# Kernel tuning notes

Measured on AMD Instinct MI355X. Metric: run time of the kernel, lower is better.

The kernel has to match this reference:

```python
import jax, jax.numpy as jnp
import numpy as np

N_NODES = 50000
N_EDGES = 1600000
D = 128


def setup_inputs() -> dict:
    key = jax.random.key(0)
    k1, k2, k3, k4 = jax.random.split(key, 4)
    x = jax.random.normal(k1, (N_NODES, D), dtype=jnp.float32)
    src = jax.random.randint(k2, (N_EDGES,), 0, N_NODES, dtype=jnp.int64)
    dst = jax.random.randint(k3, (N_EDGES,), 0, N_NODES, dtype=jnp.int64)
    # Linear(2*D, 1): weight [2*D, 1] (transposed vs torch), bias [1]
    W = jax.random.normal(k4, (2 * D, 1), dtype=jnp.float32) * (1.0 / np.sqrt(2 * D))
    b = jnp.zeros((1,), dtype=jnp.float32)
    return {"x": x, "src": src, "dst": dst, "W": W, "b": b}


def reference(x, src, dst, W, b):
    # score_e = W^T [x[src_e]; x[dst_e]] + b
    # Equivalent split form avoids materializing the [E, 2D] concat when possible,
    # but stays mathematically identical to cat + Linear.
    Ws, Wd = W[:D], W[D:]            # [D,1] each
    xs = x @ Ws                       # [N,1] per-node src contribution
    xd = x @ Wd                       # [N,1] per-node dst contribution
    score = xs[src] + xd[dst] + b     # [E,1]
    return score
```

## Files before the change

### kernel.cpp

```cpp
#include <hip/hip_runtime.h>
#include <hip/hip_bf16.h>

#define DDIM 128
#define K2_BLOCKS 256
#define K2_THREADS 1024
#define MAX_TAB32 25088

typedef float vf4 __attribute__((ext_vector_type(4)));
typedef int   vi4 __attribute__((ext_vector_type(4)));

__device__ __forceinline__ float bf16_to_f32(unsigned short u) {
    return __uint_as_float(((unsigned int)u) << 16);
}

__global__ __launch_bounds__(256) void node_proj_kernel(
    const float* __restrict__ x,
    const float* __restrict__ W,
    __hip_bfloat16* __restrict__ xs,
    __hip_bfloat16* __restrict__ xd,
    int n_nodes)
{
    const int tib    = threadIdx.x;
    const int lane   = tib & 63;
    const int wid    = blockIdx.x * (256 / 64) + (tib >> 6);
    const int nwaves = gridDim.x * (256 / 64);
    const int lc     = lane & 31;
    const int half   = lane >> 5;

    const vf4 ws4 = *reinterpret_cast<const vf4*>(W + lc * 4);
    const vf4 wd4 = *reinterpret_cast<const vf4*>(W + DDIM + lc * 4);

    const int npairs = n_nodes >> 1;
    for (int p = wid; p < npairs; p += nwaves) {
        const int row = 2 * p + half;
        const vf4 xv = __builtin_nontemporal_load(
            reinterpret_cast<const vf4*>(x + (size_t)row * DDIM + lc * 4));
        float s = xv.x * ws4.x + xv.y * ws4.y + xv.z * ws4.z + xv.w * ws4.w;
        float d = xv.x * wd4.x + xv.y * wd4.y + xv.z * wd4.z + xv.w * wd4.w;
        #pragma unroll
        for (int m = 16; m >= 1; m >>= 1) {
            s += __shfl_xor(s, m, 64);
            d += __shfl_xor(d, m, 64);
        }
        if (lc == 0) {
            xs[row] = __float2bfloat16(s);
            xd[row] = __float2bfloat16(d);
        }
    }
    if ((n_nodes & 1) && wid == 0 && half == 0) {
        const int row = n_nodes - 1;
        const vf4 xv = *reinterpret_cast<const vf4*>(
            x + (size_t)row * DDIM + lc * 4);
        float s = xv.x * ws4.x + xv.y * ws4.y + xv.z * ws4.z + xv.w * ws4.w;
        float d = xv.x * wd4.x + xv.y * wd4.y + xv.z * wd4.z + xv.w * wd4.w;
        #pragma unroll
        for (int m = 16; m >= 1; m >>= 1) {
            s += __shfl_xor(s, m, 64);
            d += __shfl_xor(d, m, 64);
        }
        if (lc == 0) {
            xs[row] = __float2bfloat16(s);
            xd[row] = __float2bfloat16(d);
        }
    }
}

__global__ __launch_bounds__(K2_THREADS) void edge_lds_kernel(
    const int* __restrict__ src,
    const int* __restrict__ dst,
    const unsigned int* __restrict__ xs32,
    const unsigned int* __restrict__ xd32,
    const float* __restrict__ b,
    float* __restrict__ out,
    int n_nodes, int n_quads, int n_edges)
{
    __shared__ unsigned short tab[MAX_TAB32 * 2];
    unsigned int* tab32 = reinterpret_cast<unsigned int*>(tab);

    const int tid = threadIdx.x;
    const int gid = blockIdx.x * K2_THREADS + tid;
    const int T   = K2_BLOCKS * K2_THREADS;
    const int n32 = (n_nodes + 1) >> 1;
    const float bb = b[0];

    for (int i = tid; i < n32; i += K2_THREADS) tab32[i] = xs32[i];
    __syncthreads();

    const int q0 = gid, q1 = gid + T;
    const bool h0 = q0 < n_quads, h1 = q1 < n_quads;
    vi4 t0 = {0,0,0,0}, t1 = {0,0,0,0};
    vf4 p0 = {0,0,0,0}, p1 = {0,0,0,0};
    if (h0) {
        const vi4 s = __builtin_nontemporal_load(
            reinterpret_cast<const vi4*>(src) + q0);
        t0 = __builtin_nontemporal_load(
            reinterpret_cast<const vi4*>(dst) + q0);
        p0.x = bf16_to_f32(tab[s.x]) + bb;
        p0.y = bf16_to_f32(tab[s.y]) + bb;
        p0.z = bf16_to_f32(tab[s.z]) + bb;
        p0.w = bf16_to_f32(tab[s.w]) + bb;
    }
    if (h1) {
        const vi4 s = __builtin_nontemporal_load(
            reinterpret_cast<const vi4*>(src) + q1);
        t1 = __builtin_nontemporal_load(
            reinterpret_cast<const vi4*>(dst) + q1);
        p1.x = bf16_to_f32(tab[s.x]) + bb;
        p1.y = bf16_to_f32(tab[s.y]) + bb;
        p1.z = bf16_to_f32(tab[s.z]) + bb;
        p1.w = bf16_to_f32(tab[s.w]) + bb;
    }
    const int tail = n_edges & 3;
    int te = -1; float pt = 0.f; int td = 0;
    if (blockIdx.x == 0 && tid < tail) {
        te = (n_quads << 2) + tid;
        td = dst[te];
        pt = bf16_to_f32(tab[src[te]]) + bb;
    }

    __syncthreads();
    for (int i = tid; i < n32; i += K2_THREADS) tab32[i] = xd32[i];
    __syncthreads();

    if (h0) {
        vf4 o;
        o.x = p0.x + bf16_to_f32(tab[t0.x]);
        o.y = p0.y + bf16_to_f32(tab[t0.y]);
        o.z = p0.z + bf16_to_f32(tab[t0.z]);
        o.w = p0.w + bf16_to_f32(tab[t0.w]);
        __builtin_nontemporal_store(o, reinterpret_cast<vf4*>(out) + q0);
    }
    if (h1) {
        vf4 o;
        o.x = p1.x + bf16_to_f32(tab[t1.x]);
        o.y = p1.y + bf16_to_f32(tab[t1.y]);
        o.z = p1.z + bf16_to_f32(tab[t1.z]);
        o.w = p1.w + bf16_to_f32(tab[t1.w]);
        __builtin_nontemporal_store(o, reinterpret_cast<vf4*>(out) + q1);
    }
    if (te >= 0) out[te] = pt + bf16_to_f32(tab[td]);
}

extern "C" void kernel_launch(void* const* d_in, const int* in_sizes, int n_in,
                              void* d_out, int out_size, void* d_ws, size_t ws_size,
                              hipStream_t stream) {
    const float* x   = (const float*)d_in[0];
    const int*   src = (const int*)d_in[1];
    const int*   dst = (const int*)d_in[2];
    const float* W   = (const float*)d_in[3];
    const float* b   = (const float*)d_in[4];
    float* out = (float*)d_out;

    const int n_nodes = in_sizes[0] / DDIM;
    const int n_edges = in_sizes[1];

    __hip_bfloat16* xs = (__hip_bfloat16*)d_ws;
    const int n_pad = (n_nodes + 1) & ~1;
    __hip_bfloat16* xd = xs + n_pad;

    node_proj_kernel<<<2048, 256, 0, stream>>>(x, W, xs, xd, n_nodes);

    const int n_quads = n_edges >> 2;
    edge_lds_kernel<<<K2_BLOCKS, K2_THREADS, 0, stream>>>(
        src, dst, (const unsigned int*)xs, (const unsigned int*)xd, b, out,
        n_nodes, n_quads, n_edges);
}
```

Before: 18.54 us.

## Prefetch node tables into registers with 128-bit loads and widen projection rows

The edge kernel now issues 128-bit loads of both the xs and xd bf16 tables into registers up front, together with the src/dst index loads, then copies them into LDS. This overlaps the global latency of the second table fill with the first gather phase, and fills LDS with wider transactions. The node projection kernel processes four rows per wave with 16 lanes each and 8 floats per lane, which shortens the shuffle reduction. The cost is higher register pressure (14 vi4 per thread at 1024 threads), which can lower occupancy or cause spills, and the xd buffer is now padded to a multiple of 8 for alignment.

```diff
diff --git a/kernel.cpp b/kernel.cpp
--- a/kernel.cpp
+++ b/kernel.cpp
@@ -5,6 +5,7 @@
 #define K2_BLOCKS 256
 #define K2_THREADS 1024
 #define MAX_TAB32 25088
+#define XD_REGS 7
 
 typedef float vf4 __attribute__((ext_vector_type(4)));
 typedef int   vi4 __attribute__((ext_vector_type(4)));
@@ -24,41 +25,53 @@
     const int lane   = tib & 63;
     const int wid    = blockIdx.x * (256 / 64) + (tib >> 6);
     const int nwaves = gridDim.x * (256 / 64);
-    const int lc     = lane & 31;
-    const int half   = lane >> 5;
-
-    const vf4 ws4 = *reinterpret_cast<const vf4*>(W + lc * 4);
-    const vf4 wd4 = *reinterpret_cast<const vf4*>(W + DDIM + lc * 4);
-
-    const int npairs = n_nodes >> 1;
-    for (int p = wid; p < npairs; p += nwaves) {
-        const int row = 2 * p + half;
-        const vf4 xv = __builtin_nontemporal_load(
-            reinterpret_cast<const vf4*>(x + (size_t)row * DDIM + lc * 4));
-        float s = xv.x * ws4.x + xv.y * ws4.y + xv.z * ws4.z + xv.w * ws4.w;
-        float d = xv.x * wd4.x + xv.y * wd4.y + xv.z * wd4.z + xv.w * wd4.w;
+    const int c      = lane & 15;
+    const int r      = lane >> 4;
+
+    const vf4 wsA = *reinterpret_cast<const vf4*>(W + c * 8);
+    const vf4 wsB = *reinterpret_cast<const vf4*>(W + c * 8 + 4);
+    const vf4 wdA = *reinterpret_cast<const vf4*>(W + DDIM + c * 8);
+    const vf4 wdB = *reinterpret_cast<const vf4*>(W + DDIM + c * 8 + 4);
+
+    const int nq = n_nodes >> 2;
+    for (int q = wid; q < nq; q += nwaves) {
+        const int row = 4 * q + r;
+        const vf4* xp = reinterpret_cast<const vf4*>(x + (size_t)row * DDIM + c * 8);
+        const vf4 xa = __builtin_nontemporal_load(xp);
+        const vf4 xb = __builtin_nontemporal_load(xp + 1);
+        float s = xa.x*wsA.x + xa.y*wsA.y + xa.z*wsA.z + xa.w*wsA.w
+                + xb.x*wsB.x + xb.y*wsB.y + xb.z*wsB.z + xb.w*wsB.w;
+        float d = xa.x*wdA.x + xa.y*wdA.y + xa.z*wdA.z + xa.w*wdA.w
+                + xb.x*wdB.x + xb.y*wdB.y + xb.z*wdB.z + xb.w*wdB.w;
         #pragma unroll
-        for (int m = 16; m >= 1; m >>= 1) {
+        for (int m = 8; m >= 1; m >>= 1) {
             s += __shfl_xor(s, m, 64);
             d += __shfl_xor(d, m, 64);
         }
-        if (lc == 0) {
+        if (c == 0) {
             xs[row] = __float2bfloat16(s);
             xd[row] = __float2bfloat16(d);
         }
     }
-    if ((n_nodes & 1) && wid == 0 && half == 0) {
-        const int row = n_nodes - 1;
-        const vf4 xv = *reinterpret_cast<const vf4*>(
-            x + (size_t)row * DDIM + lc * 4);
-        float s = xv.x * ws4.x + xv.y * ws4.y + xv.z * ws4.z + xv.w * ws4.w;
-        float d = xv.x * wd4.x + xv.y * wd4.y + xv.z * wd4.z + xv.w * wd4.w;
+    const int tail0 = nq << 2;
+    if (wid == 0 && tail0 < n_nodes) {
+        const int row = tail0 + r;
+        float s = 0.f, d = 0.f;
+        if (row < n_nodes) {
+            const vf4* xp = reinterpret_cast<const vf4*>(x + (size_t)row * DDIM + c * 8);
+            const vf4 xa = *xp;
+            const vf4 xb = *(xp + 1);
+            s = xa.x*wsA.x + xa.y*wsA.y + xa.z*wsA.z + xa.w*wsA.w
+              + xb.x*wsB.x + xb.y*wsB.y + xb.z*wsB.z + xb.w*wsB.w;
+            d = xa.x*wdA.x + xa.y*wdA.y + xa.z*wdA.z + xa.w*wdA.w
+              + xb.x*wdB.x + xb.y*wdB.y + xb.z*wdB.z + xb.w*wdB.w;
+        }
         #pragma unroll
-        for (int m = 16; m >= 1; m >>= 1) {
+        for (int m = 8; m >= 1; m >>= 1) {
             s += __shfl_xor(s, m, 64);
             d += __shfl_xor(d, m, 64);
         }
-        if (lc == 0) {
+        if (c == 0 && row < n_nodes) {
             xs[row] = __float2bfloat16(s);
             xd[row] = __float2bfloat16(d);
         }
@@ -74,41 +87,67 @@
     float* __restrict__ out,
     int n_nodes, int n_quads, int n_edges)
 {
-    __shared__ unsigned short tab[MAX_TAB32 * 2];
-    unsigned int* tab32 = reinterpret_cast<unsigned int*>(tab);
-
-    const int tid = threadIdx.x;
-    const int gid = blockIdx.x * K2_THREADS + tid;
-    const int T   = K2_BLOCKS * K2_THREADS;
-    const int n32 = (n_nodes + 1) >> 1;
-    const float bb = b[0];
-
-    for (int i = tid; i < n32; i += K2_THREADS) tab32[i] = xs32[i];
-    __syncthreads();
-
+    __shared__ __align__(16) unsigned short tab[MAX_TAB32 * 2];
+    unsigned int* tab32  = reinterpret_cast<unsigned int*>(tab);
+    vi4*          tab128 = reinterpret_cast<vi4*>(tab);
+
+    const int tid  = threadIdx.x;
+    const int gid  = blockIdx.x * K2_THREADS + tid;
+    const int T    = K2_BLOCKS * K2_THREADS;
+    const int n32  = (n_nodes + 1) >> 1;
+    const int n128 = n32 >> 2;
+    const vi4* xs128 = reinterpret_cast<const vi4*>(xs32);
+    const vi4* xd128 = reinterpret_cast<const vi4*>(xd32);
+
+    vi4 xsreg[XD_REGS];
+    #pragma unroll
+    for (int k = 0; k < XD_REGS; ++k) {
+        const int i = tid + k * K2_THREADS;
+        if (i < n128) xsreg[k] = xs128[i];
+    }
     const int q0 = gid, q1 = gid + T;
     const bool h0 = q0 < n_quads, h1 = q1 < n_quads;
+    vi4 s0 = {0,0,0,0}, s1 = {0,0,0,0};
     vi4 t0 = {0,0,0,0}, t1 = {0,0,0,0};
+    if (h0) {
+        s0 = __builtin_nontemporal_load(reinterpret_cast<const vi4*>(src) + q0);
+        t0 = __builtin_nontemporal_load(reinterpret_cast<const vi4*>(dst) + q0);
+    }
+    if (h1) {
+        s1 = __builtin_nontemporal_load(reinterpret_cast<const vi4*>(src) + q1);
+        t1 = __builtin_nontemporal_load(reinterpret_cast<const vi4*>(dst) + q1);
+    }
+    vi4 xdreg[XD_REGS];
+    #pragma unroll
+    for (int k = 0; k < XD_REGS; ++k) {
+        const int i = tid + k * K2_THREADS;
+        if (i < n128) xdreg[k] = xd128[i];
+    }
+    const float bb = b[0];
+
+    #pragma unroll
+    for (int k = 0; k < XD_REGS; ++k) {
+        const int i = tid + k * K2_THREADS;
+        if (i < n128) tab128[i] = xsreg[k];
+    }
+    for (int i = tid + XD_REGS * K2_THREADS; i < n128; i += K2_THREADS)
+        tab128[i] = xs128[i];
+    for (int i = (n128 << 2) + tid; i < n32; i += K2_THREADS)
+        tab32[i] = xs32[i];
+    __syncthreads();
+
     vf4 p0 = {0,0,0,0}, p1 = {0,0,0,0};
     if (h0) {
-        const vi4 s = __builtin_nontemporal_load(
-            reinterpret_cast<const vi4*>(src) + q0);
-        t0 = __builtin_nontemporal_load(
-            reinterpret_cast<const vi4*>(dst) + q0);
-        p0.x = bf16_to_f32(tab[s.x]) + bb;
-        p0.y = bf16_to_f32(tab[s.y]) + bb;
-        p0.z = bf16_to_f32(tab[s.z]) + bb;
-        p0.w = bf16_to_f32(tab[s.w]) + bb;
+        p0.x = bf16_to_f32(tab[s0.x]) + bb;
+        p0.y = bf16_to_f32(tab[s0.y]) + bb;
+        p0.z = bf16_to_f32(tab[s0.z]) + bb;
+        p0.w = bf16_to_f32(tab[s0.w]) + bb;
     }
     if (h1) {
-        const vi4 s = __builtin_nontemporal_load(
-            reinterpret_cast<const vi4*>(src) + q1);
-        t1 = __builtin_nontemporal_load(
-            reinterpret_cast<const vi4*>(dst) + q1);
-        p1.x = bf16_to_f32(tab[s.x]) + bb;
-        p1.y = bf16_to_f32(tab[s.y]) + bb;
-        p1.z = bf16_to_f32(tab[s.z]) + bb;
-        p1.w = bf16_to_f32(tab[s.w]) + bb;
+        p1.x = bf16_to_f32(tab[s1.x]) + bb;
+        p1.y = bf16_to_f32(tab[s1.y]) + bb;
+        p1.z = bf16_to_f32(tab[s1.z]) + bb;
+        p1.w = bf16_to_f32(tab[s1.w]) + bb;
     }
     const int tail = n_edges & 3;
     int te = -1; float pt = 0.f; int td = 0;
@@ -119,7 +158,15 @@
     }
 
     __syncthreads();
-    for (int i = tid; i < n32; i += K2_THREADS) tab32[i] = xd32[i];
+    #pragma unroll
+    for (int k = 0; k < XD_REGS; ++k) {
+        const int i = tid + k * K2_THREADS;
+        if (i < n128) tab128[i] = xdreg[k];
+    }
+    for (int i = tid + XD_REGS * K2_THREADS; i < n128; i += K2_THREADS)
+        tab128[i] = xd128[i];
+    for (int i = (n128 << 2) + tid; i < n32; i += K2_THREADS)
+        tab32[i] = xd32[i];
     __syncthreads();
 
     if (h0) {
@@ -155,7 +202,7 @@
     const int n_edges = in_sizes[1];
 
     __hip_bfloat16* xs = (__hip_bfloat16*)d_ws;
-    const int n_pad = (n_nodes + 1) & ~1;
+    const int n_pad = (n_nodes + 7) & ~7;
     __hip_bfloat16* xd = xs + n_pad;
 
     node_proj_kernel<<<2048, 256, 0, stream>>>(x, W, xs, xd, n_nodes);
```

Result: slower. 69.94 us (+277.2%).
